# Performance work log

Hardware: AMD Instinct MI355X
Metric: run time of the kernel (lower is better)

Reference implementation:

```python
import jax, jax.numpy as jnp
import numpy as np

HIDDEN = 128
IN_DIM = 2
OUT_DIM = 3


def _graph_conv(x, src, dst, edge_weight, W_rel, b_rel, W_root, num_nodes):
    # PyG GraphConv: lin_rel(scatter_add(ew * x[src] -> dst)) + lin_root(x)
    msg = x[src] * edge_weight[:, None]                       # [E, C_in]
    aggr = jax.ops.segment_sum(msg, dst, num_segments=num_nodes)  # [N, C_in]
    return aggr @ W_rel + b_rel + x @ W_root                  # [N, C_out]


def setup_inputs() -> dict:
    key = jax.random.key(0)
    ks = jax.random.split(key, 12)
    N, E = 100000, 1600000
    x = jax.random.normal(ks[0], (N, IN_DIM), dtype=jnp.float32)
    edge_index = jax.random.randint(ks[1], (2, E), 0, N, dtype=jnp.int64)
    edge_weight = jax.random.uniform(ks[2], (E,), dtype=jnp.float32)
    batch = jnp.zeros((N,), dtype=jnp.int64)

    def glorot(k, fan_in, fan_out):
        s = jnp.sqrt(1.0 / fan_in).astype(jnp.float32)
        return jax.random.uniform(k, (fan_in, fan_out), jnp.float32, -s, s)

    params = {
        "W1_rel": glorot(ks[3], IN_DIM, HIDDEN),
        "b1_rel": jnp.zeros((HIDDEN,), jnp.float32),
        "W1_root": glorot(ks[4], IN_DIM, HIDDEN),
        "W2_rel": glorot(ks[5], HIDDEN, HIDDEN),
        "b2_rel": jnp.zeros((HIDDEN,), jnp.float32),
        "W2_root": glorot(ks[6], HIDDEN, HIDDEN),
        "W3_rel": glorot(ks[7], HIDDEN, OUT_DIM),
        "b3_rel": jnp.zeros((OUT_DIM,), jnp.float32),
        "W3_root": glorot(ks[8], HIDDEN, OUT_DIM),
    }
    return {"x": x, "edge_index": edge_index, "edge_weight": edge_weight,
            "batch": batch, **params}


def reference(x, edge_index, edge_weight, batch,
              W1_rel, b1_rel, W1_root,
              W2_rel, b2_rel, W2_root,
              W3_rel, b3_rel, W3_root):
    N = x.shape[0]
    src, dst = edge_index[0], edge_index[1]
    h = _graph_conv(x, src, dst, edge_weight, W1_rel, b1_rel, W1_root, N)
    h = jax.nn.relu(h)
    h = _graph_conv(h, src, dst, edge_weight, W2_rel, b2_rel, W2_root, N)
    h = jax.nn.relu(h)
    h = _graph_conv(h, src, dst, edge_weight, W3_rel, b3_rel, W3_root, N)
    return h
```

## Files before the change

kernel.cpp:

```cpp
#include <hip/hip_runtime.h>

#define HIDDEN 128
#define NCHUNK 256
#define CBITS  9

typedef float v2f __attribute__((ext_vector_type(2)));
typedef short short8 __attribute__((ext_vector_type(8)));
typedef float f32x4 __attribute__((ext_vector_type(4)));
__device__ __forceinline__ v2f v2s(float a) { v2f r; r.x = a; r.y = a; return r; }

__device__ __forceinline__ ushort f2bf(float f) {
    uint u = __float_as_uint(f);
    u += 0x7FFFu + ((u >> 16) & 1u);
    return (ushort)(u >> 16);
}
__device__ __forceinline__ float bf2f(ushort h) {
    return __uint_as_float(((uint)h) << 16);
}

__global__ __launch_bounds__(256)
void k_bhist(const int* __restrict__ dst, int* __restrict__ bh, int E, int CS) {
    __shared__ int h[256];
    int c = blockIdx.x;
    h[threadIdx.x] = 0;
    __syncthreads();
    int beg = c * CS, end = min(E, beg + CS);
    for (int e = beg + threadIdx.x; e < end; e += 256)
        atomicAdd(&h[dst[e] >> CBITS], 1);
    __syncthreads();
    bh[c * 256 + threadIdx.x] = h[threadIdx.x];
}

__global__ __launch_bounds__(256)
void k_cscan(const int* __restrict__ bh, int* __restrict__ choff,
             int* __restrict__ bbase) {
    __shared__ int sm[256];
    int b = threadIdx.x;
    int acc = 0;
    for (int c = 0; c < NCHUNK; c += 8) {
        int v[8];
#pragma unroll
        for (int i = 0; i < 8; ++i) v[i] = bh[(c + i) * 256 + b];
#pragma unroll
        for (int i = 0; i < 8; ++i) { choff[(c + i) * 256 + b] = acc; acc += v[i]; }
    }
    int tot = acc;
    sm[b] = tot;
    __syncthreads();
    int run = tot;
    for (int d = 1; d < 256; d <<= 1) {
        int t = (b >= d) ? sm[b - d] : 0;
        __syncthreads();
        run += t;
        sm[b] = run;
        __syncthreads();
    }
    bbase[b] = run - tot;
    if (b == 255) bbase[256] = run;
}

__global__ __launch_bounds__(256)
void k_scatter(const int* __restrict__ src, const int* __restrict__ dst,
               const float* __restrict__ ew, const int* __restrict__ choff,
               const int* __restrict__ bbase, int2* __restrict__ staged,
               int E, int CS) {
    __shared__ int cur[256];
    int c = blockIdx.x;
    cur[threadIdx.x] = bbase[threadIdx.x] + choff[c * 256 + threadIdx.x];
    __syncthreads();
    int beg = c * CS, end = min(E, beg + CS);
    for (int e = beg + threadIdx.x; e < end; e += 256) {
        int d = dst[e];
        int slot = atomicAdd(&cur[d >> CBITS], 1);
        int2 p;
        p.x = src[e] | ((d & 511) << 17);
        p.y = __float_as_int(ew[e]);
        staged[slot] = p;
    }
}

__global__ __launch_bounds__(512)
void k_fine(const int2* __restrict__ staged, const int* __restrict__ bbase,
            const float* __restrict__ x,
            int* __restrict__ offs, int2* __restrict__ cpack,
            float4* __restrict__ yv, int N) {
    __shared__ int fc[512];
    __shared__ int fo[512];
    __shared__ int sm[512];
    __shared__ float agg[1024];
    int b = blockIdx.x;
    int t = threadIdx.x;
    int ebeg = bbase[b], eend = bbase[b + 1];
    fc[t] = 0;
    agg[t] = 0.f;
    agg[t + 512] = 0.f;
    __syncthreads();
    for (int e = ebeg + t; e < eend; e += 512)
        atomicAdd(&fc[(staged[e].x >> 17) & 511], 1);
    __syncthreads();
    int v = fc[t];
    sm[t] = v;
    __syncthreads();
    int run = v;
    for (int d = 1; d < 512; d <<= 1) {
        int u = (t >= d) ? sm[t - d] : 0;
        __syncthreads();
        run += u;
        sm[t] = run;
        __syncthreads();
    }
    fo[t] = run - v;
    __syncthreads();
    int nb0 = b << CBITS;
    int node = nb0 + t;
    if (node < N) offs[node] = ebeg + fo[t];
    __syncthreads();
    for (int e = ebeg + t; e < eend; e += 512) {
        int2 p = staged[e];
        int dl = (p.x >> 17) & 511;
        int srcn = p.x & 0x1FFFF;
        float w = __int_as_float(p.y);
        int ls = atomicAdd(&fo[dl], 1);
        int2 q2;
        q2.x = srcn;
        q2.y = p.y;
        cpack[ebeg + ls] = q2;
        float2 xv = *reinterpret_cast<const float2*>(x + (size_t)srcn * 2);
        atomicAdd(&agg[dl * 2 + 0], w * xv.x);
        atomicAdd(&agg[dl * 2 + 1], w * xv.y);
    }
    __syncthreads();
    if (node < N) {
        float2 xi = *reinterpret_cast<const float2*>(x + (size_t)node * 2);
        yv[node] = make_float4(agg[2 * t], agg[2 * t + 1], xi.x, xi.y);
    }
}

__device__ __forceinline__ int end_of(const int* offs, int i, int N, int E) {
    return (i + 1 < N) ? offs[i + 1] : E;
}

#define EDGE4(sK, wK)                                              \
    {                                                              \
        v2f t = B + v2s((sK).x) * WR0 + v2s((sK).y) * WR1          \
                  + v2s((sK).z) * WO0 + v2s((sK).w) * WO1;         \
        t = __builtin_elementwise_max(t, Z);                       \
        acc = acc + v2s(wK) * t;                                   \
    }

__global__ __launch_bounds__(256)
void k_gatherfused(const int* __restrict__ offs, const int2* __restrict__ cpack,
                   const float4* __restrict__ yv,
                   const float* __restrict__ W1rel, const float* __restrict__ b1,
                   const float* __restrict__ W1root,
                   ushort* __restrict__ a_hi, ushort* __restrict__ a_lo,
                   int N, int E) {
    int wv   = (blockIdx.x * 256 + threadIdx.x) >> 6;
    int lane = threadIdx.x & 63;
    if (wv >= N) return;
    wv = __builtin_amdgcn_readfirstlane(wv);

    const int c0 = lane * 2;
    const v2f WR0 = *reinterpret_cast<const v2f*>(W1rel  + c0);
    const v2f WR1 = *reinterpret_cast<const v2f*>(W1rel  + HIDDEN + c0);
    const v2f WO0 = *reinterpret_cast<const v2f*>(W1root + c0);
    const v2f WO1 = *reinterpret_cast<const v2f*>(W1root + HIDDEN + c0);
    const v2f B   = *reinterpret_cast<const v2f*>(b1 + c0);
    const v2f Z   = {0.f, 0.f};

    int start = offs[wv];
    int end   = (wv + 1 < N) ? offs[wv + 1] : E;
    v2f acc = {0.f, 0.f};

    for (int base = start; base < end; base += 64) {
        int nb = min(64, end - base);
        int sx = 0, wb = 0;
        if (lane < nb) {
            int2 p = cpack[base + lane];
            sx = p.x; wb = p.y;
        }
        int k = 0;
        for (; k + 8 <= nb; k += 8) {
            int s0 = __builtin_amdgcn_readlane(sx, k + 0);
            int s1 = __builtin_amdgcn_readlane(sx, k + 1);
            int s2 = __builtin_amdgcn_readlane(sx, k + 2);
            int s3 = __builtin_amdgcn_readlane(sx, k + 3);
            int s4 = __builtin_amdgcn_readlane(sx, k + 4);
            int s5 = __builtin_amdgcn_readlane(sx, k + 5);
            int s6 = __builtin_amdgcn_readlane(sx, k + 6);
            int s7 = __builtin_amdgcn_readlane(sx, k + 7);
            float4 y0 = yv[s0]; float4 y1 = yv[s1];
            float4 y2 = yv[s2]; float4 y3 = yv[s3];
            float4 y4 = yv[s4]; float4 y5 = yv[s5];
            float4 y6 = yv[s6]; float4 y7 = yv[s7];
            float w0 = __int_as_float(__builtin_amdgcn_readlane(wb, k + 0));
            float w1 = __int_as_float(__builtin_amdgcn_readlane(wb, k + 1));
            float w2 = __int_as_float(__builtin_amdgcn_readlane(wb, k + 2));
            float w3 = __int_as_float(__builtin_amdgcn_readlane(wb, k + 3));
            float w4 = __int_as_float(__builtin_amdgcn_readlane(wb, k + 4));
            float w5 = __int_as_float(__builtin_amdgcn_readlane(wb, k + 5));
            float w6 = __int_as_float(__builtin_amdgcn_readlane(wb, k + 6));
            float w7 = __int_as_float(__builtin_amdgcn_readlane(wb, k + 7));
            EDGE4(y0, w0) EDGE4(y1, w1) EDGE4(y2, w2) EDGE4(y3, w3)
            EDGE4(y4, w4) EDGE4(y5, w5) EDGE4(y6, w6) EDGE4(y7, w7)
        }
        for (; k + 4 <= nb; k += 4) {
            int s0 = __builtin_amdgcn_readlane(sx, k + 0);
            int s1 = __builtin_amdgcn_readlane(sx, k + 1);
            int s2 = __builtin_amdgcn_readlane(sx, k + 2);
            int s3 = __builtin_amdgcn_readlane(sx, k + 3);
            float4 y0 = yv[s0]; float4 y1 = yv[s1];
            float4 y2 = yv[s2]; float4 y3 = yv[s3];
            float w0 = __int_as_float(__builtin_amdgcn_readlane(wb, k + 0));
            float w1 = __int_as_float(__builtin_amdgcn_readlane(wb, k + 1));
            float w2 = __int_as_float(__builtin_amdgcn_readlane(wb, k + 2));
            float w3 = __int_as_float(__builtin_amdgcn_readlane(wb, k + 3));
            EDGE4(y0, w0) EDGE4(y1, w1) EDGE4(y2, w2) EDGE4(y3, w3)
        }
        for (; k < nb; ++k) {
            int s0 = __builtin_amdgcn_readlane(sx, k);
            float4 y0 = yv[s0];
            float w0 = __int_as_float(__builtin_amdgcn_readlane(wb, k));
            EDGE4(y0, w0)
        }
    }

    {
        ushort hx = f2bf(acc.x);
        ushort lx = f2bf(acc.x - bf2f(hx));
        ushort hy = f2bf(acc.y);
        ushort ly = f2bf(acc.y - bf2f(hy));
        ushort2 hv2; hv2.x = hx; hv2.y = hy;
        ushort2 lv2; lv2.x = lx; lv2.y = ly;
        *reinterpret_cast<ushort2*>(a_hi + (size_t)wv * HIDDEN + c0) = hv2;
        *reinterpret_cast<ushort2*>(a_lo + (size_t)wv * HIDDEN + c0) = lv2;
    }
}

__global__ __launch_bounds__(256)
void k_splitw(const float* __restrict__ Wrel, const float* __restrict__ Wroot,
              ushort* __restrict__ wThi, ushort* __restrict__ wTlo) {
    int idx = blockIdx.x * 256 + threadIdx.x;
    int k = idx >> 7;
    int n = idx & 127;
    float v = (k < 128) ? Wrel[(size_t)k * HIDDEN + n]
                        : Wroot[(size_t)(k - 128) * HIDDEN + n];
    ushort hb = f2bf(v);
    ushort lb = f2bf(v - bf2f(hb));
    wThi[(size_t)n * 256 + k] = hb;
    wTlo[(size_t)n * 256 + k] = lb;
}

#define BM2 64
#define W3_STRIDE 7
#define XS_LD 40

__global__ __launch_bounds__(256)
void k_node2(const ushort* __restrict__ a_hi, const ushort* __restrict__ a_lo,
             const float4* __restrict__ yv,
             const float* __restrict__ W1rel, const float* __restrict__ b1,
             const float* __restrict__ W1root,
             const ushort* __restrict__ wThi, const ushort* __restrict__ wTlo,
             const float* __restrict__ b,
             const float* __restrict__ W3rel, const float* __restrict__ b3,
             const float* __restrict__ W3root,
             float* __restrict__ z, float* __restrict__ out, int N) {
    __shared__ __align__(16) ushort Xhi[BM2 * XS_LD];
    __shared__ __align__(16) ushort Xlo[BM2 * XS_LD];
    __shared__ __align__(16) ushort Whi[HIDDEN * XS_LD];
    __shared__ __align__(16) ushort Wlo[HIDDEN * XS_LD];
    __shared__ float W3s[HIDDEN * W3_STRIDE];
    __shared__ __align__(16) float W1s[5 * HIDDEN];

    const int tid  = threadIdx.x;
    const int lane = tid & 63;
    const int wid  = tid >> 6;
    const int ci   = lane & 15;
    const int kb   = lane >> 4;
    const int nb   = blockIdx.x * BM2;

    if (tid < HIDDEN) {
#pragma unroll
        for (int c = 0; c < 3; ++c) {
            W3s[tid * W3_STRIDE + c]     = W3rel [tid * 3 + c];
            W3s[tid * W3_STRIDE + 3 + c] = W3root[tid * 3 + c];
        }
        W1s[0 * HIDDEN + tid] = b1[tid];
        W1s[1 * HIDDEN + tid] = W1rel[tid];
        W1s[2 * HIDDEN + tid] = W1rel[HIDDEN + tid];
        W1s[3 * HIDDEN + tid] = W1root[tid];
        W1s[4 * HIDDEN + tid] = W1root[HIDDEN + tid];
    }

    f32x4 acc[8];
#pragma unroll
    for (int tile = 0; tile < 8; ++tile) {
        float bb = b[tile * 16 + ci];
        f32x4 v; v[0] = bb; v[1] = bb; v[2] = bb; v[3] = bb;
        acc[tile] = v;
    }

    const int sr  = tid >> 2;
    const int skq = (tid & 3) * 8;

    for (int t = 0; t < 8; ++t) {
        const int kc = (t & 3) * 32;

        __syncthreads();
        if (t < 4) {
            int gr = nb + sr; if (gr >= N) gr = N - 1;
            size_t gofs = (size_t)gr * HIDDEN + kc + skq;
            *reinterpret_cast<short8*>(&Xhi[sr * XS_LD + skq]) =
                *reinterpret_cast<const short8*>(a_hi + gofs);
            *reinterpret_cast<short8*>(&Xlo[sr * XS_LD + skq]) =
                *reinterpret_cast<const short8*>(a_lo + gofs);
        } else {
            int gr = nb + sr; if (gr >= N) gr = N - 1;
            float4 y = yv[gr];
#pragma unroll
            for (int g = 0; g < 2; ++g) {
                int cc = kc + skq + g * 4;
                float4 bb = *reinterpret_cast<const float4*>(&W1s[0 * HIDDEN + cc]);
                float4 r0 = *reinterpret_cast<const float4*>(&W1s[1 * HIDDEN + cc]);
                float4 r1 = *reinterpret_cast<const float4*>(&W1s[2 * HIDDEN + cc]);
                float4 o0 = *reinterpret_cast<const float4*>(&W1s[3 * HIDDEN + cc]);
                float4 o1 = *reinterpret_cast<const float4*>(&W1s[4 * HIDDEN + cc]);
                float v0 = fmaf(y.x, r0.x, bb.x); v0 = fmaf(y.y, r1.x, v0);
                v0 = fmaf(y.z, o0.x, v0); v0 = fmaf(y.w, o1.x, v0); v0 = fmaxf(v0, 0.f);
                float v1 = fmaf(y.x, r0.y, bb.y); v1 = fmaf(y.y, r1.y, v1);
                v1 = fmaf(y.z, o0.y, v1); v1 = fmaf(y.w, o1.y, v1); v1 = fmaxf(v1, 0.f);
                float v2 = fmaf(y.x, r0.z, bb.z); v2 = fmaf(y.y, r1.z, v2);
                v2 = fmaf(y.z, o0.z, v2); v2 = fmaf(y.w, o1.z, v2); v2 = fmaxf(v2, 0.f);
                float v3 = fmaf(y.x, r0.w, bb.w); v3 = fmaf(y.y, r1.w, v3);
                v3 = fmaf(y.z, o0.w, v3); v3 = fmaf(y.w, o1.w, v3); v3 = fmaxf(v3, 0.f);
                ushort4 hu, lu;
                hu.x = f2bf(v0); lu.x = f2bf(v0 - bf2f(hu.x));
                hu.y = f2bf(v1); lu.y = f2bf(v1 - bf2f(hu.y));
                hu.z = f2bf(v2); lu.z = f2bf(v2 - bf2f(hu.z));
                hu.w = f2bf(v3); lu.w = f2bf(v3 - bf2f(hu.w));
                *reinterpret_cast<ushort4*>(&Xhi[sr * XS_LD + skq + g * 4]) = hu;
                *reinterpret_cast<ushort4*>(&Xlo[sr * XS_LD + skq + g * 4]) = lu;
            }
        }
#pragma unroll
        for (int q = 0; q < 2; ++q) {
            int idx = q * 256 + tid;
            int n  = idx >> 2;
            int kq = (idx & 3) * 8;
            size_t g = (size_t)n * 256 + t * 32 + kq;
            *reinterpret_cast<short8*>(&Whi[n * XS_LD + kq]) =
                *reinterpret_cast<const short8*>(wThi + g);
            *reinterpret_cast<short8*>(&Wlo[n * XS_LD + kq]) =
                *reinterpret_cast<const short8*>(wTlo + g);
        }
        __syncthreads();

        int rl = wid * 16 + ci;
        short8 afh = *reinterpret_cast<const short8*>(&Xhi[rl * XS_LD + kb * 8]);
        short8 afl = *reinterpret_cast<const short8*>(&Xlo[rl * XS_LD + kb * 8]);
#pragma unroll
        for (int tile = 0; tile < 8; ++tile) {
            int nl = tile * 16 + ci;
            short8 bfh = *reinterpret_cast<const short8*>(&Whi[nl * XS_LD + kb * 8]);
            short8 bfl = *reinterpret_cast<const short8*>(&Wlo[nl * XS_LD + kb * 8]);
            acc[tile] = __builtin_amdgcn_mfma_f32_16x16x32_bf16(afh, bfh, acc[tile], 0, 0, 0);
            acc[tile] = __builtin_amdgcn_mfma_f32_16x16x32_bf16(afh, bfl, acc[tile], 0, 0, 0);
            acc[tile] = __builtin_amdgcn_mfma_f32_16x16x32_bf16(afl, bfh, acc[tile], 0, 0, 0);
        }
    }

    const float b30 = b3[0], b31 = b3[1], b32 = b3[2];
#pragma unroll
    for (int m = 0; m < 4; ++m) {
        int node = nb + wid * 16 + kb * 4 + m;
        float zr0 = 0.f, zr1 = 0.f, zr2 = 0.f;
        float zo0 = 0.f, zo1 = 0.f, zo2 = 0.f;
#pragma unroll
        for (int tile = 0; tile < 8; ++tile) {
            float hv = fmaxf(acc[tile][m], 0.f);
            const float* w3 = &W3s[(tile * 16 + ci) * W3_STRIDE];
            zr0 = fmaf(hv, w3[0], zr0); zr1 = fmaf(hv, w3[1], zr1); zr2 = fmaf(hv, w3[2], zr2);
            zo0 = fmaf(hv, w3[3], zo0); zo1 = fmaf(hv, w3[4], zo1); zo2 = fmaf(hv, w3[5], zo2);
        }
#pragma unroll
        for (int d = 8; d >= 1; d >>= 1) {
            zr0 += __shfl_down(zr0, d, 16);
            zr1 += __shfl_down(zr1, d, 16);
            zr2 += __shfl_down(zr2, d, 16);
            zo0 += __shfl_down(zo0, d, 16);
            zo1 += __shfl_down(zo1, d, 16);
            zo2 += __shfl_down(zo2, d, 16);
        }
        if (ci == 0 && node < N) {
            z[(size_t)node * 3 + 0] = zr0;
            z[(size_t)node * 3 + 1] = zr1;
            z[(size_t)node * 3 + 2] = zr2;
            out[(size_t)node * 3 + 0] = zo0 + b30;
            out[(size_t)node * 3 + 1] = zo1 + b31;
            out[(size_t)node * 3 + 2] = zo2 + b32;
        }
    }
}

__global__ __launch_bounds__(256)
void k_gather3(const int* __restrict__ offs, const int2* __restrict__ cpack,
               const float* __restrict__ z, float* __restrict__ out,
               int N, int E) {
    int i = blockIdx.x * 256 + threadIdx.x;
    if (i >= N) return;
    int start = offs[i], end = end_of(offs, i, N, E);
    float a0 = 0.f, a1 = 0.f, a2 = 0.f;
    for (int j = start; j < end; ++j) {
        int2  p = cpack[j];
        int   s = p.x;
        float w = __int_as_float(p.y);
        const float* zp = z + (size_t)s * 3;
        a0 = fmaf(w, zp[0], a0);
        a1 = fmaf(w, zp[1], a1);
        a2 = fmaf(w, zp[2], a2);
    }
    out[(size_t)i * 3 + 0] += a0;
    out[(size_t)i * 3 + 1] += a1;
    out[(size_t)i * 3 + 2] += a2;
}

extern "C" void kernel_launch(void* const* d_in, const int* in_sizes, int n_in,
                              void* d_out, int out_size, void* d_ws, size_t ws_size,
                              hipStream_t stream) {
    const float* x      = (const float*)d_in[0];
    const int*   ei     = (const int*)  d_in[1];
    const float* ew     = (const float*)d_in[2];
    const float* W1rel  = (const float*)d_in[4];
    const float* b1     = (const float*)d_in[5];
    const float* W1root = (const float*)d_in[6];
    const float* W2rel  = (const float*)d_in[7];
    const float* b2     = (const float*)d_in[8];
    const float* W2root = (const float*)d_in[9];
    const float* W3rel  = (const float*)d_in[10];
    const float* b3     = (const float*)d_in[11];
    const float* W3root = (const float*)d_in[12];
    float* out = (float*)d_out;

    const int N = in_sizes[0] / 2;
    const int E = in_sizes[2];
    const int* src = ei;
    const int* dst = ei + E;

    ushort* hregion = (ushort*)d_ws;
    ushort* a_hi = hregion + 2 * (size_t)N * HIDDEN;
    ushort* a_lo = a_hi + (size_t)N * HIDDEN;
    int*   offs = (int*)(a_lo + (size_t)N * HIDDEN);
    size_t cpo  = (size_t)(offs + N - (int*)d_ws);
    cpo = (cpo + 1) & ~(size_t)1;
    int2*   cpack = (int2*)((int*)d_ws + cpo);
    size_t yvo  = (size_t)((char*)(cpack + E) - (char*)d_ws);
    yvo = (yvo + 15) & ~(size_t)15;
    float4* yv  = (float4*)((char*)d_ws + yvo);

    int2* staged = (int2*)d_ws;
    float* z = (float*)d_ws;
    size_t wto = ((size_t)N * 3 * sizeof(float) + 63) & ~(size_t)63;
    ushort* wThi = (ushort*)((char*)d_ws + wto);
    ushort* wTlo = wThi + 128 * 256;
    int*  bh     = (int*)a_hi;
    int*  choff  = bh + 256 * 256;
    int*  bbase  = choff + 256 * 256;

    const int CS = (E + NCHUNK - 1) / NCHUNK;
    const int NB = (N + 511) >> CBITS;

    k_bhist  <<<NCHUNK, 256, 0, stream>>>(dst, bh, E, CS);
    k_cscan  <<<1, 256, 0, stream>>>(bh, choff, bbase);
    k_scatter<<<NCHUNK, 256, 0, stream>>>(src, dst, ew, choff, bbase, staged, E, CS);
    k_fine   <<<NB, 512, 0, stream>>>(staged, bbase, x, offs, cpack, yv, N);

    {
        long long threads = (long long)N * 64;
        k_gatherfused<<<(int)((threads + 255) / 256), 256, 0, stream>>>(
            offs, cpack, yv, W1rel, b1, W1root, a_hi, a_lo, N, E);
    }

    k_splitw<<<128, 256, 0, stream>>>(W2rel, W2root, wThi, wTlo);

    k_node2<<<(N + BM2 - 1) / BM2, 256, 0, stream>>>(
        a_hi, a_lo, yv, W1rel, b1, W1root, wThi, wTlo,
        b2, W3rel, b3, W3root, z, out, N);

    k_gather3<<<(N + 255) / 256, 256, 0, stream>>>(offs, cpack, z, out, N, E);
}
```

Before: 191.2 us.

## Rewrite final gather as per-bucket edge-parallel LDS atomic aggregation

The layer-3 gather no longer assigns one thread per destination node walking its CSR segment. One 512-thread block now handles each 512-node bucket, striding over the bucket's edges and accumulating into shared memory with atomics. To support this, the compacted edge array now keeps the destination-local id packed in the high bits of the source field, and the layer-1 gather masks it out. This removes load imbalance and uncoalesced per-thread edge walks, at the cost of LDS atomic contention and a possibly misaligned float2 load from z.

```diff
diff --git a/kernel.cpp b/kernel.cpp
--- a/kernel.cpp
+++ b/kernel.cpp
@@ -121,10 +121,7 @@
         int srcn = p.x & 0x1FFFF;
         float w = __int_as_float(p.y);
         int ls = atomicAdd(&fo[dl], 1);
-        int2 q2;
-        q2.x = srcn;
-        q2.y = p.y;
-        cpack[ebeg + ls] = q2;
+        cpack[ebeg + ls] = p;
         float2 xv = *reinterpret_cast<const float2*>(x + (size_t)srcn * 2);
         atomicAdd(&agg[dl * 2 + 0], w * xv.x);
         atomicAdd(&agg[dl * 2 + 1], w * xv.y);
@@ -181,14 +178,14 @@
         }
         int k = 0;
         for (; k + 8 <= nb; k += 8) {
-            int s0 = __builtin_amdgcn_readlane(sx, k + 0);
-            int s1 = __builtin_amdgcn_readlane(sx, k + 1);
-            int s2 = __builtin_amdgcn_readlane(sx, k + 2);
-            int s3 = __builtin_amdgcn_readlane(sx, k + 3);
-            int s4 = __builtin_amdgcn_readlane(sx, k + 4);
-            int s5 = __builtin_amdgcn_readlane(sx, k + 5);
-            int s6 = __builtin_amdgcn_readlane(sx, k + 6);
-            int s7 = __builtin_amdgcn_readlane(sx, k + 7);
+            int s0 = __builtin_amdgcn_readlane(sx, k + 0) & 0x1FFFF;
+            int s1 = __builtin_amdgcn_readlane(sx, k + 1) & 0x1FFFF;
+            int s2 = __builtin_amdgcn_readlane(sx, k + 2) & 0x1FFFF;
+            int s3 = __builtin_amdgcn_readlane(sx, k + 3) & 0x1FFFF;
+            int s4 = __builtin_amdgcn_readlane(sx, k + 4) & 0x1FFFF;
+            int s5 = __builtin_amdgcn_readlane(sx, k + 5) & 0x1FFFF;
+            int s6 = __builtin_amdgcn_readlane(sx, k + 6) & 0x1FFFF;
+            int s7 = __builtin_amdgcn_readlane(sx, k + 7) & 0x1FFFF;
             float4 y0 = yv[s0]; float4 y1 = yv[s1];
             float4 y2 = yv[s2]; float4 y3 = yv[s3];
             float4 y4 = yv[s4]; float4 y5 = yv[s5];
@@ -205,10 +202,10 @@
             EDGE4(y4, w4) EDGE4(y5, w5) EDGE4(y6, w6) EDGE4(y7, w7)
         }
         for (; k + 4 <= nb; k += 4) {
-            int s0 = __builtin_amdgcn_readlane(sx, k + 0);
-            int s1 = __builtin_amdgcn_readlane(sx, k + 1);
-            int s2 = __builtin_amdgcn_readlane(sx, k + 2);
-            int s3 = __builtin_amdgcn_readlane(sx, k + 3);
+            int s0 = __builtin_amdgcn_readlane(sx, k + 0) & 0x1FFFF;
+            int s1 = __builtin_amdgcn_readlane(sx, k + 1) & 0x1FFFF;
+            int s2 = __builtin_amdgcn_readlane(sx, k + 2) & 0x1FFFF;
+            int s3 = __builtin_amdgcn_readlane(sx, k + 3) & 0x1FFFF;
             float4 y0 = yv[s0]; float4 y1 = yv[s1];
             float4 y2 = yv[s2]; float4 y3 = yv[s3];
             float w0 = __int_as_float(__builtin_amdgcn_readlane(wb, k + 0));
@@ -218,7 +215,7 @@
             EDGE4(y0, w0) EDGE4(y1, w1) EDGE4(y2, w2) EDGE4(y3, w3)
         }
         for (; k < nb; ++k) {
-            int s0 = __builtin_amdgcn_readlane(sx, k);
+            int s0 = __builtin_amdgcn_readlane(sx, k) & 0x1FFFF;
             float4 y0 = yv[s0];
             float w0 = __int_as_float(__builtin_amdgcn_readlane(wb, k));
             EDGE4(y0, w0)
@@ -402,26 +399,37 @@
     }
 }
 
-__global__ __launch_bounds__(256)
+__global__ __launch_bounds__(512)
 void k_gather3(const int* __restrict__ offs, const int2* __restrict__ cpack,
                const float* __restrict__ z, float* __restrict__ out,
-               int N, int E) {
-    int i = blockIdx.x * 256 + threadIdx.x;
-    if (i >= N) return;
-    int start = offs[i], end = end_of(offs, i, N, E);
-    float a0 = 0.f, a1 = 0.f, a2 = 0.f;
-    for (int j = start; j < end; ++j) {
-        int2  p = cpack[j];
-        int   s = p.x;
+               int N, int E, int NB) {
+    __shared__ float agg3[512 * 3];
+    int b = blockIdx.x;
+    int t = threadIdx.x;
+    agg3[t] = 0.f; agg3[t + 512] = 0.f; agg3[t + 1024] = 0.f;
+    __syncthreads();
+    int nb0 = b << CBITS;
+    int ebeg = offs[nb0];
+    int eend = (b + 1 < NB) ? offs[(b + 1) << CBITS] : E;
+    for (int e = ebeg + t; e < eend; e += 512) {
+        int2 p = cpack[e];
+        int dl = (p.x >> 17) & 511;
+        int srcn = p.x & 0x1FFFF;
         float w = __int_as_float(p.y);
-        const float* zp = z + (size_t)s * 3;
-        a0 = fmaf(w, zp[0], a0);
-        a1 = fmaf(w, zp[1], a1);
-        a2 = fmaf(w, zp[2], a2);
-    }
-    out[(size_t)i * 3 + 0] += a0;
-    out[(size_t)i * 3 + 1] += a1;
-    out[(size_t)i * 3 + 2] += a2;
+        const float* zp = z + (size_t)srcn * 3;
+        float2 z01 = *reinterpret_cast<const float2*>(zp);
+        float z2 = zp[2];
+        atomicAdd(&agg3[dl * 3 + 0], w * z01.x);
+        atomicAdd(&agg3[dl * 3 + 1], w * z01.y);
+        atomicAdd(&agg3[dl * 3 + 2], w * z2);
+    }
+    __syncthreads();
+    int node = nb0 + t;
+    if (node < N) {
+        out[(size_t)node * 3 + 0] += agg3[t * 3 + 0];
+        out[(size_t)node * 3 + 1] += agg3[t * 3 + 1];
+        out[(size_t)node * 3 + 2] += agg3[t * 3 + 2];
+    }
 }
 
 extern "C" void kernel_launch(void* const* d_in, const int* in_sizes, int n_in,
@@ -486,5 +494,5 @@
         a_hi, a_lo, yv, W1rel, b1, W1root, wThi, wTlo,
         b2, W3rel, b3, W3root, z, out, N);
 
-    k_gather3<<<(N + 255) / 256, 256, 0, stream>>>(offs, cpack, z, out, N, E);
-}
+    k_gather3<<<NB, 512, 0, stream>>>(offs, cpack, z, out, N, E, NB);
+}
```

Result: slower. 212.9 us (+11.4%).
